# Performance work log

Hardware: AMD Instinct MI355X
Metric: run time of the kernel (lower is better)

## Reference

```python
import jax, jax.numpy as jnp
import numpy as np

WEIGHT = 1.0
SIM_THRESHOLD = 0.8


def setup_inputs() -> dict:
    key = jax.random.key(0)
    k1, k2, k3, k4 = jax.random.split(key, 4)
    B, E, H, C = 8192, 16, 1024, 128  # batch, num_experts, hidden, clusters
    routing_probs = jax.random.normal(k1, (B, E), dtype=jnp.float32)
    # Clustered embeddings so some pairs exceed the similarity threshold:
    # intra-cluster cosine sim ~ 1024/(1024 + 0.09*1024) ~ 0.92 > 0.8.
    centers = jax.random.normal(k2, (C, H), dtype=jnp.float32)
    assign = jax.random.randint(k3, (B,), 0, C)
    input_embeddings = centers[assign] + 0.3 * jax.random.normal(k4, (B, H), dtype=jnp.float32)
    return {"routing_probs": routing_probs, "input_embeddings": input_embeddings}


def reference(routing_probs, input_embeddings):
    B = routing_probs.shape[0]
    # L2-normalize embeddings and build pairwise cosine similarity [B, B]
    emb = input_embeddings / jnp.linalg.norm(input_embeddings, axis=-1, keepdims=True)
    sim = emb @ emb.T
    mask = (sim > SIM_THRESHOLD) & ~jnp.eye(B, dtype=bool)
    # Batch-wide softmax/log_softmax computed once (fuses the per-pair loop)
    L = jax.nn.log_softmax(routing_probs, axis=-1)  # [B, E]
    P = jnp.exp(L)                                   # [B, E]
    neg_entropy = jnp.sum(P * L, axis=-1)            # [B], sum_k p_j log p_j
    # kl[i, j] = KL(P_j || P_i) = sum_k P_j (log P_j - L_i)
    kl = neg_entropy[None, :] - L @ P.T              # [B, B]
    cnt = jnp.sum(mask)
    loss = jnp.where(
        cnt > 0,
        jnp.sum(jnp.where(mask, kl, 0.0)) / jnp.maximum(cnt, 1).astype(kl.dtype),
        jnp.array(0.0, dtype=kl.dtype),
    )
    return WEIGHT * loss
```

## Files before the change

kernel.cpp:

```cpp
#include <hip/hip_runtime.h>
#include <hip/hip_bf16.h>
#include <math.h>

#define B_SZ 8192
#define H_SZ 1024
#define E_SZ 16
#define SIM_THR_I 12903
typedef float floatx4 __attribute__((ext_vector_type(4)));
typedef int   intx4   __attribute__((ext_vector_type(4)));

#define OFF_NE   4096
#define OFF_L    65536
#define OFF_P    (65536 + 524288)
#define OFF_EMB  2097152


__device__ __forceinline__ void gload16(const void* g, void* l) {
    __builtin_amdgcn_global_load_lds(
        (const __attribute__((address_space(1))) void*)g,
        (__attribute__((address_space(3))) void*)l, 16, 0, 0);
}

__device__ __forceinline__ unsigned int pack4_i8(float4 v, float s) {
    int a = (int)rintf(v.x * s), b = (int)rintf(v.y * s);
    int c = (int)rintf(v.z * s), d = (int)rintf(v.w * s);
    return (a & 255) | ((b & 255) << 8) | ((c & 255) << 16) | ((d & 255) << 24);
}

__global__ __launch_bounds__(256)
void prep_kernel(const float* __restrict__ rp,
                 const float* __restrict__ emb,
                 unsigned char* __restrict__ out8,
                 float* __restrict__ L, float* __restrict__ P,
                 float* __restrict__ ne,
                 float* __restrict__ gsum, unsigned int* __restrict__ gcnt,
                 unsigned int* __restrict__ done) {
    const int b = blockIdx.x;
    const int tid = threadIdx.x;
    if (b < 512) {
        __shared__ __align__(16) unsigned char stage[16 * 1040];
        const int wave = tid >> 6, lane = tid & 63;
        const int g = b;
#pragma unroll
        for (int t = 0; t < 4; t++) {
            int r = g * 16 + wave * 4 + t;
            const float4* row4 = (const float4*)(emb + (size_t)r * H_SZ);
            float4 v0 = row4[lane * 4 + 0], v1 = row4[lane * 4 + 1];
            float4 v2 = row4[lane * 4 + 2], v3 = row4[lane * 4 + 3];
            float ss = v0.x*v0.x + v0.y*v0.y + v0.z*v0.z + v0.w*v0.w
                     + v1.x*v1.x + v1.y*v1.y + v1.z*v1.z + v1.w*v1.w
                     + v2.x*v2.x + v2.y*v2.y + v2.z*v2.z + v2.w*v2.w
                     + v3.x*v3.x + v3.y*v3.y + v3.z*v3.z + v3.w*v3.w;
#pragma unroll
            for (int off = 32; off > 0; off >>= 1) ss += __shfl_down(ss, off, 64);
            ss = __shfl(ss, 0, 64);
            float s = rsqrtf(ss) * 127.0f;
            uint4 c;
            c.x = pack4_i8(v0, s);
            c.y = pack4_i8(v1, s);
            c.z = pack4_i8(v2, s);
            c.w = pack4_i8(v3, s);
            *(uint4*)(stage + (r & 15) * 1040 + lane * 16) = c;
        }
        __syncthreads();
#pragma unroll
        for (int p = 0; p < 4; p++) {
            int d = p * 256 + tid;
            int m = d & 15;
            int c = (d >> 6) * 4 + ((d >> 4) & 3);
            uint4 v = *(const uint4*)(stage + m * 1040 + c * 16);
            *(uint4*)(out8 + (size_t)g * 16384 + (size_t)d * 16) = v;
        }
    } else {
        int i = (b - 512) * 256 + tid;
        if (i == 0) { *gsum = 0.f; *gcnt = 0u; *done = 0u; }
        if (i >= B_SZ) return;
        const float* x = rp + i * E_SZ;
        float v[E_SZ];
        float m = -INFINITY;
#pragma unroll
        for (int k = 0; k < E_SZ; k++) { v[k] = x[k]; m = fmaxf(m, v[k]); }
        float s = 0.f;
#pragma unroll
        for (int k = 0; k < E_SZ; k++) s += expf(v[k] - m);
        float lse = m + logf(s);
        float nent = 0.f;
#pragma unroll
        for (int k = 0; k < E_SZ; k++) {
            float l = v[k] - lse;
            float p = expf(l);
            L[i * E_SZ + k] = l;
            P[i * E_SZ + k] = p;
            nent += p * l;
        }
        ne[i] = nent;
    }
}

__device__ __forceinline__ int cnt_range(int lo, int hi, int r, int* first) {
    int lo2 = lo + ((r - lo) & 7);
    *first = lo2;
    return (lo2 > hi) ? 0 : ((hi - lo2) >> 3) + 1;
}

#define GRID_PER_XCD 164
__global__ __launch_bounds__(512, 4)
void sim_kl_kernel(const unsigned char* __restrict__ embL,
                   const float* __restrict__ Lm, const float* __restrict__ Pm,
                   const float* __restrict__ ne,
                   float* __restrict__ gsum, unsigned int* __restrict__ gcnt,
                   unsigned int* __restrict__ done, float* __restrict__ out) {
    __shared__ __align__(16) char As[2][16384];
    __shared__ __align__(16) char Bs[2][8192];
    __shared__ float redf[8];
    __shared__ unsigned int redc[8];

    const int x = blockIdx.x & 7;
    int s = blockIdx.x >> 3;
    int BI = 0, bj = 0;
    bool have = false;
    for (BI = 0; BI < 32; BI++) {
        int lo = 2 * BI, f1, f2;
        int n1 = (lo <= 31) ? cnt_range(lo, 31, x, &f1) : 0;
        int n2 = cnt_range(lo < 32 ? 32 : lo, 63, 7 - x, &f2);
        if (s < n1) { bj = f1 + 8 * s; have = true; break; }
        s -= n1;
        if (s < n2) { bj = f2 + 8 * s; have = true; break; }
        s -= n2;
    }

    const int tid  = threadIdx.x;
    const int lane = tid & 63;
    const int wave = tid >> 6;

    float fsum = 0.f;
    unsigned int lcnt = 0;

    if (have) {
        const int rowI = BI * 256, rowJ = bj * 128;
        const int wrg = (wave >> 1);
        const int wcg = (wave & 1);
        const int quad = lane >> 4;
        const int l16  = lane & 15;

        intx4 acc[4][4];
#pragma unroll
        for (int mi = 0; mi < 4; mi++)
#pragma unroll
            for (int ni = 0; ni < 4; ni++) {
                intx4 z = {0, 0, 0, 0};
                acc[mi][ni] = z;
            }

        const char* srcA = (const char*)embL + (size_t)(BI * 16 + 2 * wave) * 16384 + lane * 16;
        const char* srcB = (const char*)embL + (size_t)(bj * 8 + wave) * 16384 + lane * 16;
        const int aW = 2 * wave * 1024;
        const int bW = wave * 1024;

        {
            gload16(srcA,         As[0] + aW);
            gload16(srcA + 16384, As[0] + aW + 1024);
            gload16(srcB,         Bs[0] + bW);
        }

        const int aoff = wrg * 4096 + lane * 16;
        const int boff = wcg * 4096 + lane * 16;

        for (int kt = 0; kt < 16; kt++) {
            const int b = kt & 1;
            __syncthreads();
            if (kt + 1 < 16) {
                const int ko = (kt + 1) * 1024;
                gload16(srcA + ko,         As[b ^ 1] + aW);
                gload16(srcA + ko + 16384, As[b ^ 1] + aW + 1024);
                gload16(srcB + ko,         Bs[b ^ 1] + bW);
            }

            intx4 af[4], bf[4];
#pragma unroll
            for (int mi = 0; mi < 4; mi++)
                af[mi] = *(const intx4*)(As[b] + aoff + mi * 1024);
#pragma unroll
            for (int ni = 0; ni < 4; ni++)
                bf[ni] = *(const intx4*)(Bs[b] + boff + ni * 1024);
#pragma unroll
            for (int mi = 0; mi < 4; mi++)
#pragma unroll
                for (int ni = 0; ni < 4; ni++)
                    acc[mi][ni] = __builtin_amdgcn_mfma_i32_16x16x64_i8(
                        af[mi], bf[ni], acc[mi][ni], 0, 0, 0);
        }

        __syncthreads();
        unsigned short* wl = (unsigned short*)As + wave * 2048;
        int base = 0;
#pragma unroll
        for (int mi = 0; mi < 4; mi++) {
#pragma unroll
            for (int ni = 0; ni < 4; ni++) {
#pragma unroll
                for (int r = 0; r < 4; r++) {
                    int il = wrg * 64 + mi * 16 + quad * 4 + r;
                    int jl = wcg * 64 + ni * 16 + l16;
                    bool msk = (acc[mi][ni][r] > SIM_THR_I) && (rowJ + jl > rowI + il);
                    unsigned long long bal = __ballot(msk);
                    if (msk) {
                        int pos = base + __popcll(bal & ((1ull << lane) - 1ull));
                        if (pos < 2048) wl[pos] = (unsigned short)((il << 7) | jl);
                    }
                    base += __popcll(bal);
                }
            }
        }
        if (base > 2048) base = 2048;

        for (int t = lane; t < base; t += 64) {
            int e = wl[t];
            int i = rowI + (e >> 7), j = rowJ + (e & 127);
            const float4* Li4 = (const float4*)(Lm + i * E_SZ);
            const float4* Pj4 = (const float4*)(Pm + j * E_SZ);
            const float4* Lj4 = (const float4*)(Lm + j * E_SZ);
            const float4* Pi4 = (const float4*)(Pm + i * E_SZ);
            float d = 0.f, d2 = 0.f;
#pragma unroll
            for (int q = 0; q < 4; q++) {
                float4 a = Li4[q], bb = Pj4[q];
                d += a.x * bb.x + a.y * bb.y + a.z * bb.z + a.w * bb.w;
                float4 a2 = Lj4[q], b2 = Pi4[q];
                d2 += a2.x * b2.x + a2.y * b2.y + a2.z * b2.z + a2.w * b2.w;
            }
            fsum += (ne[j] - d) + (ne[i] - d2);
            lcnt += 2;
        }
    }

#pragma unroll
    for (int off = 32; off > 0; off >>= 1) {
        fsum += __shfl_down(fsum, off, 64);
        lcnt += __shfl_down(lcnt, off, 64);
    }
    if (lane == 0) { redf[wave] = fsum; redc[wave] = lcnt; }
    __syncthreads();
    if (tid == 0) {
        float sv = 0.f;
        unsigned int c = 0u;
#pragma unroll
        for (int w = 0; w < 8; w++) { sv += redf[w]; c += redc[w]; }
        if (c > 0u) {
            atomicAdd(gsum, sv);
            atomicAdd(gcnt, c);
        }
        __threadfence();
        unsigned int old = atomicAdd(done, 1u);
        if (old == gridDim.x - 1) {
            float S = atomicAdd(gsum, 0.0f);
            unsigned int C = atomicAdd(gcnt, 0u);
            out[0] = (C > 0u) ? (S / (float)C) : 0.f;
        }
    }
}

extern "C" void kernel_launch(void* const* d_in, const int* in_sizes, int n_in,
                              void* d_out, int out_size, void* d_ws, size_t ws_size,
                              hipStream_t stream) {
    const float* rp  = (const float*)d_in[0];
    const float* emb = (const float*)d_in[1];
    float* out = (float*)d_out;

    char* ws = (char*)d_ws;
    float*         gsum = (float*)(ws + 0);
    unsigned int*  gcnt = (unsigned int*)(ws + 4);
    unsigned int*  done = (unsigned int*)(ws + 8);
    float*         ne   = (float*)(ws + OFF_NE);
    float*         Lm   = (float*)(ws + OFF_L);
    float*         Pm   = (float*)(ws + OFF_P);
    unsigned char* embL = (unsigned char*)(ws + OFF_EMB);

    prep_kernel<<<512 + 32, 256, 0, stream>>>(rp, emb, embL, Lm, Pm, ne, gsum, gcnt, done);
    sim_kl_kernel<<<8 * GRID_PER_XCD, 512, 0, stream>>>(embL, Lm, Pm, ne, gsum, gcnt, done, out);
}
```

Measured before the change: 165.6 us.

## Use 256x256 upper-triangle tiles with 1024-thread blocks and staggered K phase

```diff
diff --git a/kernel.cpp b/kernel.cpp
--- a/kernel.cpp
+++ b/kernel.cpp
@@ -97,141 +97,125 @@
     }
 }
 
-__device__ __forceinline__ int cnt_range(int lo, int hi, int r, int* first) {
-    int lo2 = lo + ((r - lo) & 7);
-    *first = lo2;
-    return (lo2 > hi) ? 0 : ((hi - lo2) >> 3) + 1;
-}
-
-#define GRID_PER_XCD 164
-__global__ __launch_bounds__(512, 4)
+__global__ __launch_bounds__(1024, 2)
 void sim_kl_kernel(const unsigned char* __restrict__ embL,
                    const float* __restrict__ Lm, const float* __restrict__ Pm,
                    const float* __restrict__ ne,
                    float* __restrict__ gsum, unsigned int* __restrict__ gcnt,
                    unsigned int* __restrict__ done, float* __restrict__ out) {
-    __shared__ __align__(16) char As[2][16384];
-    __shared__ __align__(16) char Bs[2][8192];
-    __shared__ float redf[8];
-    __shared__ unsigned int redc[8];
+    __shared__ __align__(16) char smem[4][16384];
+    __shared__ float redf[16];
+    __shared__ unsigned int redc[16];
 
     const int x = blockIdx.x & 7;
     int s = blockIdx.x >> 3;
-    int BI = 0, bj = 0;
-    bool have = false;
-    for (BI = 0; BI < 32; BI++) {
-        int lo = 2 * BI, f1, f2;
-        int n1 = (lo <= 31) ? cnt_range(lo, 31, x, &f1) : 0;
-        int n2 = cnt_range(lo < 32 ? 32 : lo, 63, 7 - x, &f2);
-        if (s < n1) { bj = f1 + 8 * s; have = true; break; }
-        s -= n1;
-        if (s < n2) { bj = f2 + 8 * s; have = true; break; }
-        s -= n2;
-    }
+    const int phase = s & 15;
+    int bjs[4] = { x, x + 8, 23 - x, 31 - x };
+    int bi = 0, bj = 0;
+#pragma unroll
+    for (int t = 0; t < 4; t++) {
+        int n = bjs[t] + 1;
+        if (s < n) { bj = bjs[t]; bi = s; break; }
+        s -= n;
+    }
+    const int rowI = bi * 256, rowJ = bj * 256;
 
     const int tid  = threadIdx.x;
     const int lane = tid & 63;
     const int wave = tid >> 6;
+    const int wrg = wave >> 2;
+    const int wcg = wave & 3;
+    const int quad = lane >> 4;
+    const int l16  = lane & 15;
+
+    intx4 acc[4][4];
+#pragma unroll
+    for (int mi = 0; mi < 4; mi++)
+#pragma unroll
+        for (int ni = 0; ni < 4; ni++) {
+            intx4 z = {0, 0, 0, 0};
+            acc[mi][ni] = z;
+        }
+
+    const char* srcA = (const char*)embL + (size_t)(bi * 16 + wave) * 16384 + lane * 16;
+    const char* srcB = (const char*)embL + (size_t)(bj * 16 + wave) * 16384 + lane * 16;
+    const int gW = wave * 1024;
+
+    {
+        const int ko = phase * 1024;
+        gload16(srcA + ko, smem[0] + gW);
+        gload16(srcB + ko, smem[2] + gW);
+    }
+
+    const int aoff = wrg * 4096 + lane * 16;
+    const int boff = wcg * 4096 + lane * 16;
+
+    for (int kt = 0; kt < 16; kt++) {
+        const int b = kt & 1;
+        __syncthreads();
+        if (kt + 1 < 16) {
+            const int ko = (((kt + 1) + phase) & 15) * 1024;
+            gload16(srcA + ko, smem[b ^ 1] + gW);
+            gload16(srcB + ko, smem[2 + (b ^ 1)] + gW);
+        }
+
+        intx4 af[4], bf[4];
+#pragma unroll
+        for (int mi = 0; mi < 4; mi++)
+            af[mi] = *(const intx4*)(smem[b] + aoff + mi * 1024);
+#pragma unroll
+        for (int ni = 0; ni < 4; ni++)
+            bf[ni] = *(const intx4*)(smem[2 + b] + boff + ni * 1024);
+#pragma unroll
+        for (int mi = 0; mi < 4; mi++)
+#pragma unroll
+            for (int ni = 0; ni < 4; ni++)
+                acc[mi][ni] = __builtin_amdgcn_mfma_i32_16x16x64_i8(
+                    af[mi], bf[ni], acc[mi][ni], 0, 0, 0);
+    }
+
+    __syncthreads();
+    unsigned short* wl = (unsigned short*)smem + wave * 2048;
+    int base = 0;
+#pragma unroll
+    for (int mi = 0; mi < 4; mi++) {
+#pragma unroll
+        for (int ni = 0; ni < 4; ni++) {
+#pragma unroll
+            for (int r = 0; r < 4; r++) {
+                int il = wrg * 64 + mi * 16 + quad * 4 + r;
+                int jl = wcg * 64 + ni * 16 + l16;
+                bool msk = (acc[mi][ni][r] > SIM_THR_I) && (rowJ + jl > rowI + il);
+                unsigned long long bal = __ballot(msk);
+                if (msk) {
+                    int pos = base + __popcll(bal & ((1ull << lane) - 1ull));
+                    if (pos < 2048) wl[pos] = (unsigned short)((il << 8) | jl);
+                }
+                base += __popcll(bal);
+            }
+        }
+    }
+    if (base > 2048) base = 2048;
 
     float fsum = 0.f;
     unsigned int lcnt = 0;
-
-    if (have) {
-        const int rowI = BI * 256, rowJ = bj * 128;
-        const int wrg = (wave >> 1);
-        const int wcg = (wave & 1);
-        const int quad = lane >> 4;
-        const int l16  = lane & 15;
-
-        intx4 acc[4][4];
-#pragma unroll
-        for (int mi = 0; mi < 4; mi++)
-#pragma unroll
-            for (int ni = 0; ni < 4; ni++) {
-                intx4 z = {0, 0, 0, 0};
-                acc[mi][ni] = z;
-            }
-
-        const char* srcA = (const char*)embL + (size_t)(BI * 16 + 2 * wave) * 16384 + lane * 16;
-        const char* srcB = (const char*)embL + (size_t)(bj * 8 + wave) * 16384 + lane * 16;
-        const int aW = 2 * wave * 1024;
-        const int bW = wave * 1024;
-
-        {
-            gload16(srcA,         As[0] + aW);
-            gload16(srcA + 16384, As[0] + aW + 1024);
-            gload16(srcB,         Bs[0] + bW);
-        }
-
-        const int aoff = wrg * 4096 + lane * 16;
-        const int boff = wcg * 4096 + lane * 16;
-
-        for (int kt = 0; kt < 16; kt++) {
-            const int b = kt & 1;
-            __syncthreads();
-            if (kt + 1 < 16) {
-                const int ko = (kt + 1) * 1024;
-                gload16(srcA + ko,         As[b ^ 1] + aW);
-                gload16(srcA + ko + 16384, As[b ^ 1] + aW + 1024);
-                gload16(srcB + ko,         Bs[b ^ 1] + bW);
-            }
-
-            intx4 af[4], bf[4];
-#pragma unroll
-            for (int mi = 0; mi < 4; mi++)
-                af[mi] = *(const intx4*)(As[b] + aoff + mi * 1024);
-#pragma unroll
-            for (int ni = 0; ni < 4; ni++)
-                bf[ni] = *(const intx4*)(Bs[b] + boff + ni * 1024);
-#pragma unroll
-            for (int mi = 0; mi < 4; mi++)
-#pragma unroll
-                for (int ni = 0; ni < 4; ni++)
-                    acc[mi][ni] = __builtin_amdgcn_mfma_i32_16x16x64_i8(
-                        af[mi], bf[ni], acc[mi][ni], 0, 0, 0);
-        }
-
-        __syncthreads();
-        unsigned short* wl = (unsigned short*)As + wave * 2048;
-        int base = 0;
-#pragma unroll
-        for (int mi = 0; mi < 4; mi++) {
-#pragma unroll
-            for (int ni = 0; ni < 4; ni++) {
-#pragma unroll
-                for (int r = 0; r < 4; r++) {
-                    int il = wrg * 64 + mi * 16 + quad * 4 + r;
-                    int jl = wcg * 64 + ni * 16 + l16;
-                    bool msk = (acc[mi][ni][r] > SIM_THR_I) && (rowJ + jl > rowI + il);
-                    unsigned long long bal = __ballot(msk);
-                    if (msk) {
-                        int pos = base + __popcll(bal & ((1ull << lane) - 1ull));
-                        if (pos < 2048) wl[pos] = (unsigned short)((il << 7) | jl);
-                    }
-                    base += __popcll(bal);
-                }
-            }
-        }
-        if (base > 2048) base = 2048;
-
-        for (int t = lane; t < base; t += 64) {
-            int e = wl[t];
-            int i = rowI + (e >> 7), j = rowJ + (e & 127);
-            const float4* Li4 = (const float4*)(Lm + i * E_SZ);
-            const float4* Pj4 = (const float4*)(Pm + j * E_SZ);
-            const float4* Lj4 = (const float4*)(Lm + j * E_SZ);
-            const float4* Pi4 = (const float4*)(Pm + i * E_SZ);
-            float d = 0.f, d2 = 0.f;
-#pragma unroll
-            for (int q = 0; q < 4; q++) {
-                float4 a = Li4[q], bb = Pj4[q];
-                d += a.x * bb.x + a.y * bb.y + a.z * bb.z + a.w * bb.w;
-                float4 a2 = Lj4[q], b2 = Pi4[q];
-                d2 += a2.x * b2.x + a2.y * b2.y + a2.z * b2.z + a2.w * b2.w;
-            }
-            fsum += (ne[j] - d) + (ne[i] - d2);
-            lcnt += 2;
-        }
+    for (int t = lane; t < base; t += 64) {
+        int e = wl[t];
+        int i = rowI + (e >> 8), j = rowJ + (e & 255);
+        const float4* Li4 = (const float4*)(Lm + i * E_SZ);
+        const float4* Pj4 = (const float4*)(Pm + j * E_SZ);
+        const float4* Lj4 = (const float4*)(Lm + j * E_SZ);
+        const float4* Pi4 = (const float4*)(Pm + i * E_SZ);
+        float d = 0.f, d2 = 0.f;
+#pragma unroll
+        for (int q = 0; q < 4; q++) {
+            float4 a = Li4[q], bb = Pj4[q];
+            d += a.x * bb.x + a.y * bb.y + a.z * bb.z + a.w * bb.w;
+            float4 a2 = Lj4[q], b2 = Pi4[q];
+            d2 += a2.x * b2.x + a2.y * b2.y + a2.z * b2.z + a2.w * b2.w;
+        }
+        fsum += (ne[j] - d) + (ne[i] - d2);
+        lcnt += 2;
     }
 
 #pragma unroll
@@ -245,7 +229,7 @@
         float sv = 0.f;
         unsigned int c = 0u;
 #pragma unroll
-        for (int w = 0; w < 8; w++) { sv += redf[w]; c += redc[w]; }
+        for (int w = 0; w < 16; w++) { sv += redf[w]; c += redc[w]; }
         if (c > 0u) {
             atomicAdd(gsum, sv);
             atomicAdd(gcnt, c);
@@ -277,5 +261,5 @@
     unsigned char* embL = (unsigned char*)(ws + OFF_EMB);
 
     prep_kernel<<<512 + 32, 256, 0, stream>>>(rp, emb, embL, Lm, Pm, ne, gsum, gcnt, done);
-    sim_kl_kernel<<<8 * GRID_PER_XCD, 512, 0, stream>>>(embL, Lm, Pm, ne, gsum, gcnt, done, out);
-}
+    sim_kl_kernel<<<528, 1024, 0, stream>>>(embL, Lm, Pm, ne, gsum, gcnt, done, out);
+}
```

New measurement: 147.8 us. -10.7%, faster.
